# Optimization experiments

Measured on AMD Instinct MI355X. Metric: run time of the kernel, lower is better.

Reference implementation:

```python
import jax, jax.numpy as jnp
import numpy as np

N_HEAD = 16
NEG = -10000.0


def setup_inputs() -> dict:
    key = jax.random.key(0)
    k1, k2, k3 = jax.random.split(key, 3)
    B, S, NX = 2, 2048, 1024
    x = jax.random.normal(k1, (B, S, NX), dtype=jnp.float32)
    # Conv1D weights: y = x @ W + b (HF Conv1D stores weight as [in, out])
    w_attn = jax.random.normal(k2, (NX, 3 * NX), dtype=jnp.float32) * 0.02
    b_attn = jnp.zeros((3 * NX,), dtype=jnp.float32)
    w_proj = jax.random.normal(k3, (NX, NX), dtype=jnp.float32) * 0.02
    b_proj = jnp.zeros((NX,), dtype=jnp.float32)
    return {"x": x, "w_attn": w_attn, "b_attn": b_attn,
            "w_proj": w_proj, "b_proj": b_proj}


def reference(x, w_attn, b_attn, w_proj, b_proj):
    B, S, NX = x.shape
    H = N_HEAD
    D = NX // H  # head dim
    qkv = x @ w_attn + b_attn                      # [B, S, 3*NX]
    q, k, v = jnp.split(qkv, 3, axis=-1)
    # split heads -> [B, H, S, D]
    q = q.reshape(B, S, H, D).transpose(0, 2, 1, 3)
    k = k.reshape(B, S, H, D).transpose(0, 2, 1, 3)
    v = v.reshape(B, S, H, D).transpose(0, 2, 1, 3)
    # scores [B, H, S, S], scaled (scale=True)
    w = jnp.einsum('bhqd,bhkd->bhqk', q, k) / jnp.sqrt(jnp.asarray(D, x.dtype))
    # causal additive mask exactly as the torch code: w*b + NEG*(1-b)
    bias = jnp.tril(jnp.ones((S, S), dtype=x.dtype))[None, None]  # [1,1,S,S]
    w = w * bias + NEG * (1.0 - bias)
    w = jax.nn.softmax(w, axis=-1)
    a = jnp.einsum('bhqk,bhkd->bhqd', w, v)        # [B, H, S, D]
    a = a.transpose(0, 2, 1, 3).reshape(B, S, NX)  # merge heads
    return a @ w_proj + b_proj
```

## Files before the change

### kernel.cpp

```cpp
#include <hip/hip_runtime.h>
#include <cstdint>
#include <cstddef>


typedef __bf16 bf16;
typedef __bf16 bf16x8 __attribute__((ext_vector_type(8)));
typedef __bf16 bf16x4 __attribute__((ext_vector_type(4)));
typedef float f32x4 __attribute__((ext_vector_type(4)));

#define MFMA16(a, b, c) __builtin_amdgcn_mfma_f32_16x16x32_bf16(a, b, c, 0, 0, 0)

typedef const __attribute__((address_space(1))) void* gas_ptr;
typedef __attribute__((address_space(3))) void* las_ptr;
__device__ __forceinline__ void async16(const void* g, void* l) {
    __builtin_amdgcn_global_load_lds((gas_ptr)g, (las_ptr)l, 16, 0, 0);
}
__device__ __forceinline__ float exp2f_fast(float x) { return __builtin_amdgcn_exp2f(x); }

__global__ void cvt_kernel(const float* __restrict__ in, bf16* __restrict__ out, int n) {
    int i = (blockIdx.x * blockDim.x + threadIdx.x) * 4;
    if (i >= n) return;
    float4 v = *reinterpret_cast<const float4*>(in + i);
    bf16x4 o;
    o[0] = (bf16)v.x; o[1] = (bf16)v.y; o[2] = (bf16)v.z; o[3] = (bf16)v.w;
    *reinterpret_cast<bf16x4*>(out + i) = o;
}

__global__ void transpose_kernel(const float* __restrict__ in, bf16* __restrict__ out,
                                 int K, int N) {
    __shared__ float tile[32][33];
    int n0 = blockIdx.x * 32, k0 = blockIdx.y * 32;
    int tx = threadIdx.x, ty = threadIdx.y;
#pragma unroll
    for (int i = 0; i < 32; i += 8)
        tile[ty + i][tx] = in[(size_t)(k0 + ty + i) * N + n0 + tx];
    __syncthreads();
#pragma unroll
    for (int i = 0; i < 32; i += 8)
        out[(size_t)(n0 + ty + i) * K + k0 + tx] = (bf16)tile[tx][ty + i];
}

template <int OUT_BF16>
__global__ __launch_bounds__(256) void gemm_kernel(const bf16* __restrict__ A,
                                                   const bf16* __restrict__ Bt,
                                                   const float* __restrict__ bias,
                                                   void* __restrict__ Cout,
                                                   int M, int N, int K) {
    __shared__ bf16 Alds[2][128 * 32];
    __shared__ bf16 Blds[2][128 * 32];
    const int tid = threadIdx.x;
    const int w = tid >> 6, l = tid & 63;
    const int lane16 = l & 15, quad = l >> 4;
    const int wr = w >> 1, wc = w & 1;
    const int row0 = blockIdx.y * 128, col0 = blockIdx.x * 128;

    const int e = tid * 8;
    const int sr = e >> 5, sc = e & 31;

    f32x4 zero4 = {0.f, 0.f, 0.f, 0.f};
    f32x4 acc[4][4];
#pragma unroll
    for (int i = 0; i < 4; ++i)
#pragma unroll
        for (int j = 0; j < 4; ++j) acc[i][j] = zero4;

#pragma unroll
    for (int ch = 0; ch < 2; ++ch) {
        async16(A + (size_t)(row0 + ch * 64 + sr) * K + sc, &Alds[0][ch * 2048 + e]);
        async16(Bt + (size_t)(col0 + ch * 64 + sr) * K + sc, &Blds[0][ch * 2048 + e]);
    }

    const int niter = K >> 5;
    for (int it = 0; it < niter; ++it) {
        const int cur = it & 1;
        __syncthreads();
        if (it + 1 < niter) {
            const int k1 = (it + 1) << 5;
#pragma unroll
            for (int ch = 0; ch < 2; ++ch) {
                async16(A + (size_t)(row0 + ch * 64 + sr) * K + k1 + sc, &Alds[cur ^ 1][ch * 2048 + e]);
                async16(Bt + (size_t)(col0 + ch * 64 + sr) * K + k1 + sc, &Blds[cur ^ 1][ch * 2048 + e]);
            }
        }
        bf16x8 af[4], bfr[4];
#pragma unroll
        for (int i = 0; i < 4; ++i) {
            af[i] = *reinterpret_cast<const bf16x8*>(&Alds[cur][(64 * wr + 16 * i + lane16) * 32 + quad * 8]);
            bfr[i] = *reinterpret_cast<const bf16x8*>(&Blds[cur][(64 * wc + 16 * i + lane16) * 32 + quad * 8]);
        }
#pragma unroll
        for (int i = 0; i < 4; ++i)
#pragma unroll
            for (int j = 0; j < 4; ++j) acc[i][j] = MFMA16(af[i], bfr[j], acc[i][j]);
    }

#pragma unroll
    for (int i = 0; i < 4; ++i)
#pragma unroll
        for (int j = 0; j < 4; ++j)
#pragma unroll
            for (int r = 0; r < 4; ++r) {
                int row = row0 + 64 * wr + 16 * i + quad * 4 + r;
                int col = col0 + 64 * wc + 16 * j + lane16;
                float v = acc[i][j][r] + bias[col];
                if (OUT_BF16)
                    reinterpret_cast<bf16*>(Cout)[(size_t)row * N + col] = (bf16)v;
                else
                    reinterpret_cast<float*>(Cout)[(size_t)row * N + col] = v;
            }
}

template <int OUT_BF16>
__global__ __launch_bounds__(256) void gemm64_kernel(const bf16* __restrict__ A,
                                                     const bf16* __restrict__ Bt,
                                                     const float* __restrict__ bias,
                                                     void* __restrict__ Cout,
                                                     int M, int N, int K) {
    __shared__ bf16 Alds[2][64 * 32];
    __shared__ bf16 Blds[2][128 * 32];
    const int tid = threadIdx.x;
    const int w = tid >> 6, l = tid & 63;
    const int lane16 = l & 15, quad = l >> 4;
    const int wr = w >> 1, wc = w & 1;
    const int row0 = blockIdx.y * 64, col0 = blockIdx.x * 128;

    const int e = tid * 8;
    const int sr = e >> 5, sc = e & 31;

    f32x4 zero4 = {0.f, 0.f, 0.f, 0.f};
    f32x4 acc[2][4];
#pragma unroll
    for (int i = 0; i < 2; ++i)
#pragma unroll
        for (int j = 0; j < 4; ++j) acc[i][j] = zero4;

    async16(A + (size_t)(row0 + sr) * K + sc, &Alds[0][e]);
#pragma unroll
    for (int ch = 0; ch < 2; ++ch)
        async16(Bt + (size_t)(col0 + ch * 64 + sr) * K + sc, &Blds[0][ch * 2048 + e]);

    const int niter = K >> 5;
    for (int it = 0; it < niter; ++it) {
        const int cur = it & 1;
        __syncthreads();
        if (it + 1 < niter) {
            const int k1 = (it + 1) << 5;
            async16(A + (size_t)(row0 + sr) * K + k1 + sc, &Alds[cur ^ 1][e]);
#pragma unroll
            for (int ch = 0; ch < 2; ++ch)
                async16(Bt + (size_t)(col0 + ch * 64 + sr) * K + k1 + sc, &Blds[cur ^ 1][ch * 2048 + e]);
        }
        bf16x8 af[2], bfr[4];
#pragma unroll
        for (int i = 0; i < 2; ++i)
            af[i] = *reinterpret_cast<const bf16x8*>(&Alds[cur][(32 * wr + 16 * i + lane16) * 32 + quad * 8]);
#pragma unroll
        for (int j = 0; j < 4; ++j)
            bfr[j] = *reinterpret_cast<const bf16x8*>(&Blds[cur][(64 * wc + 16 * j + lane16) * 32 + quad * 8]);
#pragma unroll
        for (int i = 0; i < 2; ++i)
#pragma unroll
            for (int j = 0; j < 4; ++j) acc[i][j] = MFMA16(af[i], bfr[j], acc[i][j]);
    }

#pragma unroll
    for (int i = 0; i < 2; ++i)
#pragma unroll
        for (int j = 0; j < 4; ++j)
#pragma unroll
            for (int r = 0; r < 4; ++r) {
                int row = row0 + 32 * wr + 16 * i + quad * 4 + r;
                int col = col0 + 64 * wc + 16 * j + lane16;
                float v = acc[i][j][r] + bias[col];
                if (OUT_BF16)
                    reinterpret_cast<bf16*>(Cout)[(size_t)row * N + col] = (bf16)v;
                else
                    reinterpret_cast<float*>(Cout)[(size_t)row * N + col] = v;
            }
}

__global__ __launch_bounds__(256) void attn_kernel(const bf16* __restrict__ qkv,
                                                   bf16* __restrict__ aout) {
    const int S = 2048;
    const int bh = blockIdx.x;
    const int b = bh >> 4, h = bh & 15;
    const int qt = 31 - blockIdx.y;
    const int nkt = qt + 1;
    const int tid = threadIdx.x, w = tid >> 6, l = tid & 63;
    const int lane16 = l & 15, quad = l >> 4;

    __shared__ bf16 Klds[64 * 72];
    __shared__ bf16 Vt[64 * 72];
    __shared__ bf16 Plds[4][16 * 72];

    const bf16* base = qkv + (size_t)b * S * 3072;
    const float qscale = 0.125f * 1.4426950408889634f;
    const float NEGs = -10000.0f * 1.4426950408889634f;

    bf16x8 qf[2];
#pragma unroll
    for (int hv = 0; hv < 2; ++hv) {
        const bf16* qp = base + (size_t)(qt * 64 + 16 * w + lane16) * 3072 + h * 64;
        bf16x8 t = *reinterpret_cast<const bf16x8*>(qp + hv * 32 + quad * 8);
#pragma unroll
        for (int j = 0; j < 8; ++j) t[j] = (bf16)((float)t[j] * qscale);
        qf[hv] = t;
    }

    f32x4 zero4 = {0.f, 0.f, 0.f, 0.f};
    f32x4 o[4];
#pragma unroll
    for (int df = 0; df < 4; ++df) o[df] = zero4;
    float lsum = 0.f;

    const int kr = tid >> 3, kc = (tid & 7) * 8;
    const int vp = tid & 31, vd = (tid >> 5) * 8;
    bf16x8 kreg0, kreg1, vreg0, vreg1;
    auto load_tile = [&](int kt) {
        const bf16* tb = base + (size_t)(kt * 64) * 3072;
        kreg0 = *reinterpret_cast<const bf16x8*>(tb + (size_t)kr * 3072 + 1024 + h * 64 + kc);
        kreg1 = *reinterpret_cast<const bf16x8*>(tb + (size_t)(32 + kr) * 3072 + 1024 + h * 64 + kc);
        vreg0 = *reinterpret_cast<const bf16x8*>(tb + (size_t)(2 * vp) * 3072 + 2048 + h * 64 + vd);
        vreg1 = *reinterpret_cast<const bf16x8*>(tb + (size_t)(2 * vp + 1) * 3072 + 2048 + h * 64 + vd);
    };

    load_tile(0);
    for (int kt = 0; kt < nkt; ++kt) {
        __syncthreads();
        *reinterpret_cast<bf16x8*>(&Klds[kr * 72 + kc]) = kreg0;
        *reinterpret_cast<bf16x8*>(&Klds[(32 + kr) * 72 + kc]) = kreg1;
#pragma unroll
        for (int j = 0; j < 8; ++j) {
            union { bf16 h2[2]; uint32_t u; } pk;
            pk.h2[0] = vreg0[j]; pk.h2[1] = vreg1[j];
            *reinterpret_cast<uint32_t*>(&Vt[(vd + j) * 72 + 2 * vp]) = pk.u;
        }
        __syncthreads();
        if (kt + 1 < nkt) load_tile(kt + 1);

        f32x4 st[4];
#pragma unroll
        for (int kf = 0; kf < 4; ++kf) {
            bf16x8 k0 = *reinterpret_cast<const bf16x8*>(&Klds[(kf * 16 + lane16) * 72 + quad * 8]);
            bf16x8 k1 = *reinterpret_cast<const bf16x8*>(&Klds[(kf * 16 + lane16) * 72 + 32 + quad * 8]);
            f32x4 z = zero4;
            z = MFMA16(k0, qf[0], z);
            z = MFMA16(k1, qf[1], z);
            st[kf] = z;
        }

        if (kt == qt) {
            const int q = qt * 64 + 16 * w + lane16;
#pragma unroll
            for (int kf = 0; kf < 4; ++kf)
#pragma unroll
                for (int r = 0; r < 4; ++r)
                    if (kt * 64 + kf * 16 + quad * 4 + r > q) st[kf][r] = NEGs;
        }

        float rs = 0.f;
        bf16* Prow = &Plds[w][lane16 * 72];
#pragma unroll
        for (int kf = 0; kf < 4; ++kf) {
            bf16x4 pk;
#pragma unroll
            for (int r = 0; r < 4; ++r) {
                float pv = exp2f_fast(st[kf][r]);
                rs += pv;
                pk[r] = (bf16)pv;
            }
            *reinterpret_cast<bf16x4*>(Prow + kf * 16 + quad * 4) = pk;
        }
        lsum += rs;

#pragma unroll
        for (int kf2 = 0; kf2 < 2; ++kf2) {
            bf16x8 pf = *reinterpret_cast<const bf16x8*>(
                &Plds[w][lane16 * 72 + kf2 * 32 + quad * 8]);
#pragma unroll
            for (int df = 0; df < 4; ++df) {
                bf16x8 vf = *reinterpret_cast<const bf16x8*>(
                    &Vt[(df * 16 + lane16) * 72 + kf2 * 32 + quad * 8]);
                o[df] = MFMA16(pf, vf, o[df]);
            }
        }
    }

    lsum += __shfl_xor(lsum, 16, 64);
    lsum += __shfl_xor(lsum, 32, 64);
    float inv = 1.0f / lsum;

#pragma unroll
    for (int r = 0; r < 4; ++r) {
        float li = __shfl(inv, quad * 4 + r, 64);
        int row = qt * 64 + 16 * w + quad * 4 + r;
#pragma unroll
        for (int df = 0; df < 4; ++df)
            aout[(size_t)(b * S + row) * 1024 + h * 64 + df * 16 + lane16] =
                (bf16)(o[df][r] * li);
    }
}

extern "C" void kernel_launch(void* const* d_in, const int* in_sizes, int n_in,
                              void* d_out, int out_size, void* d_ws, size_t ws_size,
                              hipStream_t stream) {
    const float* x      = (const float*)d_in[0];
    const float* w_attn = (const float*)d_in[1];
    const float* b_attn = (const float*)d_in[2];
    const float* w_proj = (const float*)d_in[3];
    const float* b_proj = (const float*)d_in[4];
    float* out = (float*)d_out;
    char* ws = (char*)d_ws;

    const int Mtok = 4096, NX = 1024, N3 = 3072;
    bf16* xb   = (bf16*)(ws);
    bf16* wTa  = (bf16*)(ws + ((size_t)8 << 20));
    bf16* wTp  = (bf16*)(ws + ((size_t)14 << 20));
    bf16* qkv  = (bf16*)(ws + ((size_t)16 << 20));
    bf16* abuf = (bf16*)(ws + ((size_t)40 << 20));

    cvt_kernel<<<dim3((Mtok * NX / 4 + 255) / 256), 256, 0, stream>>>(x, xb, Mtok * NX);
    transpose_kernel<<<dim3(N3 / 32, NX / 32), dim3(32, 8), 0, stream>>>(w_attn, wTa, NX, N3);
    transpose_kernel<<<dim3(NX / 32, NX / 32), dim3(32, 8), 0, stream>>>(w_proj, wTp, NX, NX);

    gemm_kernel<1><<<dim3(N3 / 128, Mtok / 128), 256, 0, stream>>>(xb, wTa, b_attn, qkv, Mtok, N3, NX);
    attn_kernel<<<dim3(32, 32), 256, 0, stream>>>(qkv, abuf);
    gemm64_kernel<0><<<dim3(NX / 128, Mtok / 64), 256, 0, stream>>>(abuf, wTp, b_proj, out, Mtok, NX, NX);
}
```

Measured before the change: 178.3 us.

## Fuse prep kernels, deepen output-GEMM K tile with swizzle, rebalance attention tile order

Merges the input conversion and both weight transposes into one launch. The output projection GEMM now stages 64-wide K slices with an XOR-swizzled LDS layout, halving barrier count and avoiding bank conflicts. The attention grid reorders query tiles into a zigzag so heavy and light causal tiles interleave across the dispatch order. Costs are more LDS per block in the projection GEMM, which may reduce occupancy, and some divergent index arithmetic in the fused prep kernel.

```diff
diff --git a/kernel.cpp b/kernel.cpp
--- a/kernel.cpp
+++ b/kernel.cpp
@@ -17,20 +17,25 @@
 }
 __device__ __forceinline__ float exp2f_fast(float x) { return __builtin_amdgcn_exp2f(x); }
 
-__global__ void cvt_kernel(const float* __restrict__ in, bf16* __restrict__ out, int n) {
-    int i = (blockIdx.x * blockDim.x + threadIdx.x) * 4;
-    if (i >= n) return;
-    float4 v = *reinterpret_cast<const float4*>(in + i);
-    bf16x4 o;
-    o[0] = (bf16)v.x; o[1] = (bf16)v.y; o[2] = (bf16)v.z; o[3] = (bf16)v.w;
-    *reinterpret_cast<bf16x4*>(out + i) = o;
-}
-
-__global__ void transpose_kernel(const float* __restrict__ in, bf16* __restrict__ out,
-                                 int K, int N) {
+__global__ __launch_bounds__(256) void prep_kernel(const float* __restrict__ x, bf16* __restrict__ xb,
+                                                   const float* __restrict__ wa, bf16* __restrict__ wTa,
+                                                   const float* __restrict__ wp, bf16* __restrict__ wTp) {
     __shared__ float tile[32][33];
-    int n0 = blockIdx.x * 32, k0 = blockIdx.y * 32;
-    int tx = threadIdx.x, ty = threadIdx.y;
+    const int bid = blockIdx.x, tid = threadIdx.x;
+    if (bid < 4096) {
+        int i = (bid * 256 + tid) * 4;
+        float4 v = *reinterpret_cast<const float4*>(x + i);
+        bf16x4 o;
+        o[0] = (bf16)v.x; o[1] = (bf16)v.y; o[2] = (bf16)v.z; o[3] = (bf16)v.w;
+        *reinterpret_cast<bf16x4*>(xb + i) = o;
+        return;
+    }
+    const float* in; bf16* out; int N, t;
+    if (bid < 7168) { t = bid - 4096; in = wa; out = wTa; N = 3072; }
+    else            { t = bid - 7168; in = wp; out = wTp; N = 1024; }
+    const int K = 1024;
+    int bx = t % (N >> 5), by = t / (N >> 5);
+    int n0 = bx * 32, k0 = by * 32, tx = tid & 31, ty = tid >> 5;
 #pragma unroll
     for (int i = 0; i < 32; i += 8)
         tile[ty + i][tx] = in[(size_t)(k0 + ty + i) * N + n0 + tx];
@@ -111,22 +116,19 @@
 }
 
 template <int OUT_BF16>
-__global__ __launch_bounds__(256) void gemm64_kernel(const bf16* __restrict__ A,
-                                                     const bf16* __restrict__ Bt,
-                                                     const float* __restrict__ bias,
-                                                     void* __restrict__ Cout,
-                                                     int M, int N, int K) {
-    __shared__ bf16 Alds[2][64 * 32];
-    __shared__ bf16 Blds[2][128 * 32];
+__global__ __launch_bounds__(256) void gemm64k_kernel(const bf16* __restrict__ A,
+                                                      const bf16* __restrict__ Bt,
+                                                      const float* __restrict__ bias,
+                                                      void* __restrict__ Cout,
+                                                      int M, int N, int K) {
+    __shared__ bf16 Alds[2][64 * 64];
+    __shared__ bf16 Blds[2][128 * 64];
     const int tid = threadIdx.x;
     const int w = tid >> 6, l = tid & 63;
     const int lane16 = l & 15, quad = l >> 4;
     const int wr = w >> 1, wc = w & 1;
     const int row0 = blockIdx.y * 64, col0 = blockIdx.x * 128;
 
-    const int e = tid * 8;
-    const int sr = e >> 5, sc = e & 31;
-
     f32x4 zero4 = {0.f, 0.f, 0.f, 0.f};
     f32x4 acc[2][4];
 #pragma unroll
@@ -134,33 +136,52 @@
 #pragma unroll
         for (int j = 0; j < 4; ++j) acc[i][j] = zero4;
 
-    async16(A + (size_t)(row0 + sr) * K + sc, &Alds[0][e]);
-#pragma unroll
-    for (int ch = 0; ch < 2; ++ch)
-        async16(Bt + (size_t)(col0 + ch * 64 + sr) * K + sc, &Blds[0][ch * 2048 + e]);
-
-    const int niter = K >> 5;
+    auto stage = [&](int buf, int k0) {
+#pragma unroll
+        for (int c = 0; c < 2; ++c) {
+            int idx = c * 256 + tid;
+            int r = idx >> 3, cc = idx & 7, gc = cc ^ (r & 7);
+            async16(A + (size_t)(row0 + r) * K + k0 + gc * 8, &Alds[buf][idx * 8]);
+        }
+#pragma unroll
+        for (int c = 0; c < 4; ++c) {
+            int idx = c * 256 + tid;
+            int r = idx >> 3, cc = idx & 7, gc = cc ^ (r & 7);
+            async16(Bt + (size_t)(col0 + r) * K + k0 + gc * 8, &Blds[buf][idx * 8]);
+        }
+    };
+
+    stage(0, 0);
+    const int niter = K >> 6;
     for (int it = 0; it < niter; ++it) {
         const int cur = it & 1;
         __syncthreads();
-        if (it + 1 < niter) {
-            const int k1 = (it + 1) << 5;
-            async16(A + (size_t)(row0 + sr) * K + k1 + sc, &Alds[cur ^ 1][e]);
-#pragma unroll
-            for (int ch = 0; ch < 2; ++ch)
-                async16(Bt + (size_t)(col0 + ch * 64 + sr) * K + k1 + sc, &Blds[cur ^ 1][ch * 2048 + e]);
-        }
-        bf16x8 af[2], bfr[4];
-#pragma unroll
-        for (int i = 0; i < 2; ++i)
-            af[i] = *reinterpret_cast<const bf16x8*>(&Alds[cur][(32 * wr + 16 * i + lane16) * 32 + quad * 8]);
-#pragma unroll
-        for (int j = 0; j < 4; ++j)
-            bfr[j] = *reinterpret_cast<const bf16x8*>(&Blds[cur][(64 * wc + 16 * j + lane16) * 32 + quad * 8]);
-#pragma unroll
-        for (int i = 0; i < 2; ++i)
-#pragma unroll
-            for (int j = 0; j < 4; ++j) acc[i][j] = MFMA16(af[i], bfr[j], acc[i][j]);
+        if (it + 1 < niter) stage(cur ^ 1, (it + 1) << 6);
+        bf16x8 af[2][2], bfr[4][2];
+#pragma unroll
+        for (int i = 0; i < 2; ++i) {
+            int r = 32 * wr + 16 * i + lane16;
+#pragma unroll
+            for (int ks = 0; ks < 2; ++ks) {
+                int cc = (quad + 4 * ks) ^ (r & 7);
+                af[i][ks] = *reinterpret_cast<const bf16x8*>(&Alds[cur][r * 64 + cc * 8]);
+            }
+        }
+#pragma unroll
+        for (int j = 0; j < 4; ++j) {
+            int r = 64 * wc + 16 * j + lane16;
+#pragma unroll
+            for (int ks = 0; ks < 2; ++ks) {
+                int cc = (quad + 4 * ks) ^ (r & 7);
+                bfr[j][ks] = *reinterpret_cast<const bf16x8*>(&Blds[cur][r * 64 + cc * 8]);
+            }
+        }
+#pragma unroll
+        for (int ks = 0; ks < 2; ++ks)
+#pragma unroll
+            for (int i = 0; i < 2; ++i)
+#pragma unroll
+                for (int j = 0; j < 4; ++j) acc[i][j] = MFMA16(af[i][ks], bfr[j][ks], acc[i][j]);
     }
 
 #pragma unroll
@@ -184,7 +205,8 @@
     const int S = 2048;
     const int bh = blockIdx.x;
     const int b = bh >> 4, h = bh & 15;
-    const int qt = 31 - blockIdx.y;
+    const int rr = blockIdx.y >> 3, j = blockIdx.y & 7;
+    const int qt = (rr == 0) ? (31 - j) : (rr == 1) ? (16 + j) : (rr == 2) ? (15 - j) : j;
     const int nkt = qt + 1;
     const int tid = threadIdx.x, w = tid >> 6, l = tid & 63;
     const int lane16 = l & 15, quad = l >> 4;
@@ -203,7 +225,7 @@
         const bf16* qp = base + (size_t)(qt * 64 + 16 * w + lane16) * 3072 + h * 64;
         bf16x8 t = *reinterpret_cast<const bf16x8*>(qp + hv * 32 + quad * 8);
 #pragma unroll
-        for (int j = 0; j < 8; ++j) t[j] = (bf16)((float)t[j] * qscale);
+        for (int jj = 0; jj < 8; ++jj) t[jj] = (bf16)((float)t[jj] * qscale);
         qf[hv] = t;
     }
 
@@ -230,10 +252,10 @@
         *reinterpret_cast<bf16x8*>(&Klds[kr * 72 + kc]) = kreg0;
         *reinterpret_cast<bf16x8*>(&Klds[(32 + kr) * 72 + kc]) = kreg1;
 #pragma unroll
-        for (int j = 0; j < 8; ++j) {
+        for (int jj = 0; jj < 8; ++jj) {
             union { bf16 h2[2]; uint32_t u; } pk;
-            pk.h2[0] = vreg0[j]; pk.h2[1] = vreg1[j];
-            *reinterpret_cast<uint32_t*>(&Vt[(vd + j) * 72 + 2 * vp]) = pk.u;
+            pk.h2[0] = vreg0[jj]; pk.h2[1] = vreg1[jj];
+            *reinterpret_cast<uint32_t*>(&Vt[(vd + jj) * 72 + 2 * vp]) = pk.u;
         }
         __syncthreads();
         if (kt + 1 < nkt) load_tile(kt + 1);
@@ -319,11 +341,8 @@
     bf16* qkv  = (bf16*)(ws + ((size_t)16 << 20));
     bf16* abuf = (bf16*)(ws + ((size_t)40 << 20));
 
-    cvt_kernel<<<dim3((Mtok * NX / 4 + 255) / 256), 256, 0, stream>>>(x, xb, Mtok * NX);
-    transpose_kernel<<<dim3(N3 / 32, NX / 32), dim3(32, 8), 0, stream>>>(w_attn, wTa, NX, N3);
-    transpose_kernel<<<dim3(NX / 32, NX / 32), dim3(32, 8), 0, stream>>>(w_proj, wTp, NX, NX);
-
+    prep_kernel<<<dim3(8192), 256, 0, stream>>>(x, xb, w_attn, wTa, w_proj, wTp);
     gemm_kernel<1><<<dim3(N3 / 128, Mtok / 128), 256, 0, stream>>>(xb, wTa, b_attn, qkv, Mtok, N3, NX);
     attn_kernel<<<dim3(32, 32), 256, 0, stream>>>(qkv, abuf);
-    gemm64_kernel<0><<<dim3(NX / 128, Mtok / 64), 256, 0, stream>>>(abuf, wTp, b_proj, out, Mtok, NX, NX);
-}
+    gemm64k_kernel<0><<<dim3(NX / 128, Mtok / 64), 256, 0, stream>>>(abuf, wTp, b_proj, out, Mtok, NX, NX);
+}
```

Result: faster. 171.0 us (-4.1%).
